# Kernel optimization log

Measured on AMD Instinct MI355X. Metric: run time of the kernel, lower is better.

The kernel has to match this reference:

```python
import jax, jax.numpy as jnp
import numpy as np

NUM_SEG = 196  # fixed max number of segments (fill_max of segment ids)


def setup_inputs() -> dict:
    key = jax.random.key(0)
    ks = jax.random.split(key, 6)
    B, H, W = 16, 224, 224
    in_chans, inter_dim, embed_dim, k = 3, 64, 768, 7
    x = jax.random.normal(ks[0], (B, in_chans, H, W), jnp.float32)
    segment = jax.random.randint(ks[1], (B, H, W), 0, NUM_SEG, dtype=jnp.int64)
    conv1_w = jax.random.normal(ks[2], (inter_dim, in_chans, k, k), jnp.float32) * 0.02
    conv1_b = jnp.zeros((inter_dim,), jnp.float32)
    pos_embed = jax.random.normal(ks[3], (1, inter_dim, H, W), jnp.float32) * 0.02
    conv2_w = jax.random.normal(ks[4], (embed_dim, inter_dim, 3), jnp.float32) * 0.02
    conv2_b = jnp.zeros((embed_dim,), jnp.float32)
    return {"x": x, "segment": segment, "conv1_w": conv1_w, "conv1_b": conv1_b,
            "pos_embed": pos_embed, "conv2_w": conv2_w, "conv2_b": conv2_b}


def _remap(s):
    # torch.unique(return_inverse=True): map ids to ranks in sorted unique order.
    present = jnp.zeros((NUM_SEG,), jnp.int32).at[s].set(1)
    rank = jnp.cumsum(present) - 1  # rank of each possible id among present ids
    return rank[s]


def _segment_mean(hc, idx):
    # hc: [C, N], idx: [N] -> [C, NUM_SEG]; empty segments -> 0 (sum 0 / clamp 1)
    sums = jax.ops.segment_sum(hc.T, idx, num_segments=NUM_SEG)           # [S, C]
    cnt = jax.ops.segment_sum(jnp.ones(idx.shape, hc.dtype), idx,
                              num_segments=NUM_SEG)                       # [S]
    return (sums / jnp.maximum(cnt, 1.0)[:, None]).T


def reference(x, segment, conv1_w, conv1_b, pos_embed, conv2_w, conv2_b):
    # conv1, stride 1, 'same' padding (odd kernel -> SAME matches torch)
    h = jax.lax.conv_general_dilated(
        x, conv1_w, window_strides=(1, 1), padding='SAME',
        dimension_numbers=('NCHW', 'OIHW', 'NCHW')) + conv1_b[None, :, None, None]
    h = h + pos_embed
    B, C, H, W = h.shape
    # segment already at (H, W): nearest-interpolate to same size is identity
    seg = segment.reshape(B, -1).astype(jnp.int32)      # [B, H*W]
    f_segment = jax.vmap(_remap)(seg)                   # per-sample unique inverse
    pooled = jax.vmap(_segment_mean)(h.reshape(B, C, -1), f_segment)  # [B, C, S]
    # conv1d k=3, padding=1
    out = jax.lax.conv_general_dilated(
        pooled, conv2_w, window_strides=(1,), padding=[(1, 1)],
        dimension_numbers=('NCH', 'OIH', 'NCH')) + conv2_b[None, :, None]
    out = out.transpose(0, 2, 1)                        # [B, S, embed_dim]
    return out, f_segment.reshape(B, 1, H, W)
```

## Files before the change

kernel.cpp:

```cpp
#include <hip/hip_runtime.h>
#include <hip/hip_bf16.h>

constexpr int B = 16, H = 224, W = 224, CI = 3, CO = 64, K = 7;
constexpr int SEG = 196, E = 768;
constexpr int HW = H * W;
constexpr int PP = 201;
constexpr int EC = 32;

constexpr int TSLOTS = 10;
constexpr int TROW = 72;
constexpr int TX = 32;

typedef __attribute__((ext_vector_type(8))) short bf16x8;
typedef __attribute__((ext_vector_type(16))) float f32x16;

__device__ inline unsigned short bfb(float f) {
    union { __hip_bfloat16 h; unsigned short u; } cv; cv.h = __float2bfloat16(f); return cv.u;
}
__device__ inline unsigned pack2(float lo, float hi) {
    return (unsigned)bfb(lo) | ((unsigned)bfb(hi) << 16);
}
__device__ inline float bf2f(unsigned short u) {
    return __uint_as_float(((unsigned)u) << 16);
}

__global__ void k_count(const int* __restrict__ seg, int* __restrict__ present,
                        unsigned* __restrict__ counts_raw) {
    __shared__ unsigned cnt[SEG];
    const int tid = threadIdx.x, b = blockIdx.y, y0 = blockIdx.x * 8;
    for (int i = tid; i < SEG; i += 256) cnt[i] = 0u;
    __syncthreads();
    for (int i = tid; i < 8 * W; i += 256) {
        int s = seg[b * HW + y0 * W + i];
        present[b * SEG + s] = 1;
        atomicAdd(&cnt[s], 1u);
    }
    __syncthreads();
    for (int i = tid; i < SEG; i += 256)
        if (cnt[i]) atomicAdd(&counts_raw[b * SEG + i], cnt[i]);
}

__global__ void k_offsets(const int* __restrict__ present,
                          const unsigned* __restrict__ counts_raw,
                          int* __restrict__ rank, int* __restrict__ off_rank,
                          int* __restrict__ cnt_rank, unsigned* __restrict__ cursor) {
    __shared__ int buf[256];
    const int b = blockIdx.x, t = threadIdx.x;
    int pres = (t < SEG) ? present[b * SEG + t] : 0;
    int cv   = (t < SEG) ? (int)counts_raw[b * SEG + t] : 0;
    buf[t] = pres; __syncthreads();
    for (int off = 1; off < 256; off <<= 1) {
        int u = (t >= off) ? buf[t - off] : 0; __syncthreads();
        buf[t] += u; __syncthreads();
    }
    int rk = buf[t] - 1;
    if (t < SEG) rank[b * SEG + t] = rk;
    __syncthreads();
    buf[t] = cv; __syncthreads();
    for (int off = 1; off < 256; off <<= 1) {
        int u = (t >= off) ? buf[t - off] : 0; __syncthreads();
        buf[t] += u; __syncthreads();
    }
    int offx = buf[t] - cv;
    if (t < SEG) {
        cursor[b * SEG + t] = (unsigned)offx;
        cnt_rank[b * SEG + t] = 0;
        off_rank[b * SEG + t] = 0;
    }
    __syncthreads();
    if (t < SEG && pres) {
        cnt_rank[b * SEG + rk] = cv;
        off_rank[b * SEG + rk] = offx;
    }
}

__global__ void k_scatter(const int* __restrict__ seg, const int* __restrict__ rank,
                          unsigned* __restrict__ cursor, unsigned* __restrict__ bucket,
                          float* __restrict__ out2) {
    __shared__ unsigned bcnt[SEG];
    __shared__ int base_l[SEG];
    __shared__ int rank_lds[SEG];
    __shared__ unsigned char ss[8 * W];
    __shared__ unsigned short lp[8 * W];
    const int tid = threadIdx.x, b = blockIdx.y, y0 = blockIdx.x * 8;
    for (int i = tid; i < SEG; i += 256) { bcnt[i] = 0u; rank_lds[i] = rank[b * SEG + i]; }
    __syncthreads();
    for (int i = tid; i < 8 * W; i += 256) {
        int s = seg[b * HW + y0 * W + i];
        ss[i] = (unsigned char)s;
        out2[b * HW + y0 * W + i] = (float)rank_lds[s];
        lp[i] = (unsigned short)atomicAdd(&bcnt[s], 1u);
    }
    __syncthreads();
    for (int i = tid; i < SEG; i += 256)
        if (bcnt[i]) base_l[i] = (int)atomicAdd(&cursor[b * SEG + i], bcnt[i]);
    __syncthreads();
    for (int i = tid; i < 8 * W; i += 256) {
        int s = ss[i];
        bucket[b * HW + base_l[s] + lp[i]] = (unsigned)(y0 * W + i);
    }
}

__global__ void k_post(const float* __restrict__ pos, unsigned short* __restrict__ pos_t) {
    const int p = blockIdx.x * 256 + threadIdx.x;
    unsigned d[32];
    #pragma unroll
    for (int c = 0; c < 32; ++c) {
        float v0 = pos[(size_t)(2 * c) * HW + p];
        float v1 = pos[(size_t)(2 * c + 1) * HW + p];
        d[c] = pack2(v0, v1);
    }
    uint4* op = (uint4*)&pos_t[(size_t)p * 64];
    #pragma unroll
    for (int q = 0; q < 8; ++q) {
        uint4 v = {d[4 * q], d[4 * q + 1], d[4 * q + 2], d[4 * q + 3]};
        op[q] = v;
    }
}

__launch_bounds__(256, 2)
__global__ void k_conv_mfma(const float* __restrict__ x,
                            const float* __restrict__ w1,
                            const float* __restrict__ b1,
                            const unsigned short* __restrict__ pos_t,
                            __hip_bfloat16* __restrict__ h, int b0) {
    __shared__ unsigned short Tl[TSLOTS * TX * TROW];
    __shared__ unsigned short Wl[7 * 32 * 64];

    const int tid = threadIdx.x;
    const int lb  = blockIdx.x;
    const int b   = b0 + lb;
    const int x0  = blockIdx.y * 32;
    const int y0  = blockIdx.z * 28;
    const int lane = tid & 63;
    const int ln31 = lane & 31;
    const int g    = lane >> 5;

    for (int i = tid; i < TSLOTS * TX * TROW; i += 256) Tl[i] = 0;
    for (int i = tid; i < 7 * 32 * 64; i += 256) Wl[i] = 0;
    __syncthreads();

    for (int i = tid; i < CO * CI * K * K; i += 256) {
        int co = i / 147, rem = i % 147;
        int ci = rem / 49, kyx = rem % 49;
        int ky = kyx / 7, kx = kyx % 7;
        Wl[(ky * 32 + ci * 8 + kx) * 64 + co] = bfb(w1[i]);
    }

    auto build = [&](int rbase, int nrows) {
        for (int idx = tid; idx < 96 * nrows; idx += 256) {
            int j = idx / 96, rem = idx % 96;
            int ci = rem >> 5, xl = rem & 31;
            int r = rbase + j;
            unsigned slot = (unsigned)(r + 3) % TSLOTS;
            unsigned d0 = 0, d1 = 0, d2 = 0, d3 = 0;
            if (r >= 0 && r < H) {
                const float* xr = &x[((size_t)(b * CI + ci) * H + r) * W];
                float v[7];
                #pragma unroll
                for (int kx = 0; kx < 7; ++kx) {
                    int gx = x0 + xl - 3 + kx;
                    v[kx] = (gx >= 0 && gx < W) ? xr[gx] : 0.f;
                }
                d0 = pack2(v[0], v[1]); d1 = pack2(v[2], v[3]);
                d2 = pack2(v[4], v[5]); d3 = pack2(v[6], 0.f);
            }
            uint4 dv = {d0, d1, d2, d3};
            *(uint4*)&Tl[(slot * TX + xl) * TROW + ci * 8] = dv;
        }
    };

    build(y0 - 3, TSLOTS);
    __syncthreads();

    bf16x8 bfr[7][2][2];
    #pragma unroll
    for (int ky = 0; ky < 7; ++ky)
        #pragma unroll
        for (int ks = 0; ks < 2; ++ks)
            #pragma unroll
            for (int cg = 0; cg < 2; ++cg) {
                bf16x8 f;
                #pragma unroll
                for (int e = 0; e < 8; ++e)
                    f[e] = (short)Wl[(ky * 32 + ks * 16 + g * 8 + e) * 64 + cg * 32 + ln31];
                bfr[ky][ks][cg] = f;
            }
    const float b1v0 = b1[ln31];
    const float b1v1 = b1[32 + ln31];

    for (int s = 0; s < 7; ++s) {
        const int ys = y0 + s * 4;
        const int y  = ys + (tid >> 6);

        f32x16 c0 = {0.f}; f32x16 c1 = {0.f};
        #pragma unroll
        for (int i = 0; i < 16; ++i) { c0[i] = 0.f; c1[i] = 0.f; }

        #pragma unroll
        for (int ky = 0; ky < 7; ++ky) {
            unsigned slot = (unsigned)(y + ky) % TSLOTS;
            const unsigned short* trow = &Tl[slot * TX * TROW];
            #pragma unroll
            for (int ks = 0; ks < 2; ++ks) {
                bf16x8 a = *(const bf16x8*)&trow[ln31 * TROW + ks * 16 + g * 8];
                c0 = __builtin_amdgcn_mfma_f32_32x32x16_bf16(a, bfr[ky][ks][0], c0, 0, 0, 0);
                c1 = __builtin_amdgcn_mfma_f32_32x32x16_bf16(a, bfr[ky][ks][1], c1, 0, 0, 0);
            }
        }

        #pragma unroll
        for (int reg = 0; reg < 16; ++reg) {
            int pxl = (reg & 3) + 8 * (reg >> 2) + 4 * g;
            size_t p = (size_t)y * W + x0 + pxl;
            float pv0 = bf2f(pos_t[p * 64 + ln31]);
            float pv1 = bf2f(pos_t[p * 64 + 32 + ln31]);
            __hip_bfloat16* hp = &h[((size_t)lb * HW + p) * CO];
            hp[ln31]      = __float2bfloat16(c0[reg] + pv0 + b1v0);
            hp[32 + ln31] = __float2bfloat16(c1[reg] + pv1 + b1v1);
        }

        __syncthreads();
        if (s < 6) build(ys + 7, 4);
        __syncthreads();
    }
}

__global__ void k_gather(const __hip_bfloat16* __restrict__ h,
                         const unsigned* __restrict__ bucket,
                         const int* __restrict__ off_rank,
                         const int* __restrict__ cnt_rank,
                         float* __restrict__ pooled, int b0) {
    const int tid = threadIdx.x;
    const int wave = tid >> 6, lane = tid & 63;
    const int r = blockIdx.x * 4 + wave;
    const int lb = blockIdx.y, b = b0 + lb;
    const int n = cnt_rank[b * SEG + r];
    const int base = off_rank[b * SEG + r];
    const int ps = lane >> 3, cg = lane & 7;

    float acc[8] = {0.f, 0.f, 0.f, 0.f, 0.f, 0.f, 0.f, 0.f};
    const unsigned* bk = &bucket[b * HW + base];
    const int iters = (n + 7) >> 3;
    for (int i = 0; i < iters; ++i) {
        int idx = i * 8 + ps;
        if (idx < n) {
            unsigned p = bk[idx];
            uint4 u = *(const uint4*)&h[((size_t)lb * HW + p) * CO + cg * 8];
            acc[0] += __uint_as_float((u.x & 0xffffu) << 16);
            acc[1] += __uint_as_float(u.x & 0xffff0000u);
            acc[2] += __uint_as_float((u.y & 0xffffu) << 16);
            acc[3] += __uint_as_float(u.y & 0xffff0000u);
            acc[4] += __uint_as_float((u.z & 0xffffu) << 16);
            acc[5] += __uint_as_float(u.z & 0xffff0000u);
            acc[6] += __uint_as_float((u.w & 0xffffu) << 16);
            acc[7] += __uint_as_float(u.w & 0xffff0000u);
        }
    }
    #pragma unroll
    for (int m = 8; m < 64; m <<= 1)
        #pragma unroll
        for (int j = 0; j < 8; ++j) acc[j] += __shfl_xor(acc[j], m, 64);

    if (ps == 0) {
        float inv = (n > 0) ? 1.f / (float)n : 0.f;
        float* op = &pooled[((size_t)b * SEG + r) * CO + cg * 8];
        float4 v0 = {acc[0] * inv, acc[1] * inv, acc[2] * inv, acc[3] * inv};
        float4 v1 = {acc[4] * inv, acc[5] * inv, acc[6] * inv, acc[7] * inv};
        *(float4*)&op[0] = v0;
        *(float4*)&op[4] = v1;
    }
}

__launch_bounds__(256, 2)
__global__ void k_pool_conv1d(const float* __restrict__ pooledg,
                              const float* __restrict__ w2,
                              const float* __restrict__ b2,
                              float* __restrict__ out0) {
    __shared__ float pooled[CO * PP];
    __shared__ float w2l[192 * (EC + 1)];
    const int tid = threadIdx.x;
    const int b  = blockIdx.y;
    const int e0 = blockIdx.x * EC;

    for (int i = tid; i < SEG * CO; i += 256) {
        int s = i >> 6, c = i & 63;
        pooled[c * PP + s + 1] = pooledg[((size_t)b * SEG + s) * CO + c];
    }
    for (int i = tid; i < CO * 5; i += 256) {
        int c = i / 5, hh = i % 5;
        pooled[c * PP + (hh == 0 ? 0 : 196 + hh)] = 0.f;
    }
    for (int i = tid; i < EC * 192; i += 256) {
        int e = i / 192, k = i % 192;
        w2l[k * (EC + 1) + e] = w2[(size_t)(e0 + e) * 192 + k];
    }
    __syncthreads();

    const int txs = tid & 31;
    const int te  = tid >> 5;
    const int s0  = txs * 7;
    float acc[7][4];
    #pragma unroll
    for (int ss = 0; ss < 7; ++ss)
        #pragma unroll
        for (int ee = 0; ee < 4; ++ee) acc[ss][ee] = b2[e0 + te * 4 + ee];

    if (s0 < SEG) {
        #pragma unroll 4
        for (int c = 0; c < CO; ++c) {
            float pv[9];
            #pragma unroll
            for (int j = 0; j < 9; ++j) pv[j] = pooled[c * PP + s0 + j];
            #pragma unroll
            for (int dk = 0; dk < 3; ++dk) {
                float wv[4];
                #pragma unroll
                for (int ee = 0; ee < 4; ++ee)
                    wv[ee] = w2l[(c * 3 + dk) * (EC + 1) + te * 4 + ee];
                #pragma unroll
                for (int ss = 0; ss < 7; ++ss)
                    #pragma unroll
                    for (int ee = 0; ee < 4; ++ee)
                        acc[ss][ee] = fmaf(pv[ss + dk], wv[ee], acc[ss][ee]);
            }
        }
        #pragma unroll
        for (int ss = 0; ss < 7; ++ss) {
            int s = s0 + ss;
            float* op = &out0[((size_t)(b * SEG + s) * E) + e0 + te * 4];
            float4 v0 = {acc[ss][0], acc[ss][1], acc[ss][2], acc[ss][3]};
            *(float4*)op = v0;
        }
    }
}

extern "C" void kernel_launch(void* const* d_in, const int* in_sizes, int n_in,
                              void* d_out, int out_size, void* d_ws, size_t ws_size,
                              hipStream_t stream) {
    const float* x   = (const float*)d_in[0];
    const int*   seg = (const int*)d_in[1];
    const float* w1  = (const float*)d_in[2];
    const float* b1  = (const float*)d_in[3];
    const float* pos = (const float*)d_in[4];
    const float* w2  = (const float*)d_in[5];
    const float* b2  = (const float*)d_in[6];

    float* out0 = (float*)d_out;
    float* out2 = out0 + (size_t)B * SEG * E;

    int*      present    = (int*)d_ws;
    unsigned* counts_raw = (unsigned*)(present + B * SEG);
    int*      rank       = (int*)(counts_raw + B * SEG);
    int*      off_rank   = rank + B * SEG;
    int*      cnt_rank   = off_rank + B * SEG;
    unsigned* cursor     = (unsigned*)(cnt_rank + B * SEG);
    float*    pooled     = (float*)(cursor + B * SEG);
    unsigned* bucket     = (unsigned*)(pooled + (size_t)B * SEG * CO);
    unsigned short* pos_t = (unsigned short*)(bucket + (size_t)B * HW);
    __hip_bfloat16* hbuf = (__hip_bfloat16*)(pos_t + (size_t)HW * CO);

    hipMemsetAsync(d_ws, 0, (size_t)2 * B * SEG * 4, stream);

    k_post   <<<dim3(HW / 256), 256, 0, stream>>>(pos, pos_t);
    k_count  <<<dim3(28, B), 256, 0, stream>>>(seg, present, counts_raw);
    k_offsets<<<dim3(B),     256, 0, stream>>>(present, counts_raw, rank, off_rank, cnt_rank, cursor);
    k_scatter<<<dim3(28, B), 256, 0, stream>>>(seg, rank, cursor, bucket, out2);

    size_t used = (char*)hbuf - (char*)d_ws;
    size_t h_per_img = (size_t)HW * CO * sizeof(__hip_bfloat16);
    size_t avail = (ws_size > used) ? ws_size - used : 0;
    int ipc = (int)(avail / h_per_img);
    if (ipc < 1) ipc = 1;
    if (ipc > B) ipc = B;

    for (int b0 = 0; b0 < B; b0 += ipc) {
        int nb = (b0 + ipc <= B) ? ipc : (B - b0);
        k_conv_mfma<<<dim3(nb, 7, 8), 256, 0, stream>>>(x, w1, b1, pos_t, hbuf, b0);
        k_gather   <<<dim3(49, nb),   256, 0, stream>>>(hbuf, bucket, off_rank, cnt_rank, pooled, b0);
    }
    k_pool_conv1d<<<dim3(24, B), 256, 0, stream>>>(pooled, w2, b2, out0);
}
```

Before: 248.5 us.

## Pre-pack conv weights, fold bias into pos, prefetch input rows across MFMA steps

Moves the conv1 weight transpose into a small kernel that writes weights already laid out as MFMA B fragments, so each conv block loads them with vector loads and no longer needs the weight LDS array. The bias is folded into the pre-transposed positional embedding. The input tile gets a compact LDS layout, which frees shared memory and lets the launch bound rise to 3 blocks per SM. Next-row input loads are issued into registers before the MFMA loop and written to LDS after it, so global latency overlaps compute. The cost is higher register pressure from the prefetch buffers and one extra kernel launch.

```diff
diff --git a/kernel.cpp b/kernel.cpp
--- a/kernel.cpp
+++ b/kernel.cpp
@@ -8,8 +8,6 @@
 constexpr int EC = 32;
 
 constexpr int TSLOTS = 10;
-constexpr int TROW = 72;
-constexpr int TX = 32;
 
 typedef __attribute__((ext_vector_type(8))) short bf16x8;
 typedef __attribute__((ext_vector_type(16))) float f32x16;
@@ -101,13 +99,14 @@
     }
 }
 
-__global__ void k_post(const float* __restrict__ pos, unsigned short* __restrict__ pos_t) {
+__global__ void k_post(const float* __restrict__ pos, const float* __restrict__ b1,
+                       unsigned short* __restrict__ pos_t) {
     const int p = blockIdx.x * 256 + threadIdx.x;
     unsigned d[32];
     #pragma unroll
     for (int c = 0; c < 32; ++c) {
-        float v0 = pos[(size_t)(2 * c) * HW + p];
-        float v1 = pos[(size_t)(2 * c + 1) * HW + p];
+        float v0 = pos[(size_t)(2 * c) * HW + p]     + b1[2 * c];
+        float v1 = pos[(size_t)(2 * c + 1) * HW + p] + b1[2 * c + 1];
         d[c] = pack2(v0, v1);
     }
     uint4* op = (uint4*)&pos_t[(size_t)p * 64];
@@ -118,14 +117,27 @@
     }
 }
 
-__launch_bounds__(256, 2)
+__global__ void k_wt(const float* __restrict__ w1, unsigned short* __restrict__ w1t) {
+    int i = blockIdx.x * 256 + threadIdx.x;
+    if (i < 7 * 2 * 2 * 64 * 8) {
+        int e = i & 7, lane = (i >> 3) & 63, cg = (i >> 9) & 1, ks = (i >> 10) & 1, ky = i >> 11;
+        int kk = ks * 16 + (lane >> 5) * 8 + e;
+        int co = cg * 32 + (lane & 31);
+        float v = 0.f;
+        if (kk < 24) {
+            int ci = kk >> 3, kx = kk & 7;
+            if (kx < 7) v = w1[((co * 3 + ci) * 7 + ky) * 7 + kx];
+        }
+        w1t[i] = bfb(v);
+    }
+}
+
+__launch_bounds__(256, 3)
 __global__ void k_conv_mfma(const float* __restrict__ x,
-                            const float* __restrict__ w1,
-                            const float* __restrict__ b1,
+                            const unsigned short* __restrict__ w1t,
                             const unsigned short* __restrict__ pos_t,
                             __hip_bfloat16* __restrict__ h, int b0) {
-    __shared__ unsigned short Tl[TSLOTS * TX * TROW];
-    __shared__ unsigned short Wl[7 * 32 * 64];
+    __shared__ unsigned short Tl[TSLOTS * 4 * 32 * 8];
 
     const int tid = threadIdx.x;
     const int lb  = blockIdx.x;
@@ -135,43 +147,7 @@
     const int lane = tid & 63;
     const int ln31 = lane & 31;
     const int g    = lane >> 5;
-
-    for (int i = tid; i < TSLOTS * TX * TROW; i += 256) Tl[i] = 0;
-    for (int i = tid; i < 7 * 32 * 64; i += 256) Wl[i] = 0;
-    __syncthreads();
-
-    for (int i = tid; i < CO * CI * K * K; i += 256) {
-        int co = i / 147, rem = i % 147;
-        int ci = rem / 49, kyx = rem % 49;
-        int ky = kyx / 7, kx = kyx % 7;
-        Wl[(ky * 32 + ci * 8 + kx) * 64 + co] = bfb(w1[i]);
-    }
-
-    auto build = [&](int rbase, int nrows) {
-        for (int idx = tid; idx < 96 * nrows; idx += 256) {
-            int j = idx / 96, rem = idx % 96;
-            int ci = rem >> 5, xl = rem & 31;
-            int r = rbase + j;
-            unsigned slot = (unsigned)(r + 3) % TSLOTS;
-            unsigned d0 = 0, d1 = 0, d2 = 0, d3 = 0;
-            if (r >= 0 && r < H) {
-                const float* xr = &x[((size_t)(b * CI + ci) * H + r) * W];
-                float v[7];
-                #pragma unroll
-                for (int kx = 0; kx < 7; ++kx) {
-                    int gx = x0 + xl - 3 + kx;
-                    v[kx] = (gx >= 0 && gx < W) ? xr[gx] : 0.f;
-                }
-                d0 = pack2(v[0], v[1]); d1 = pack2(v[2], v[3]);
-                d2 = pack2(v[4], v[5]); d3 = pack2(v[6], 0.f);
-            }
-            uint4 dv = {d0, d1, d2, d3};
-            *(uint4*)&Tl[(slot * TX + xl) * TROW + ci * 8] = dv;
-        }
-    };
-
-    build(y0 - 3, TSLOTS);
-    __syncthreads();
+    const int wave = tid >> 6;
 
     bf16x8 bfr[7][2][2];
     #pragma unroll
@@ -179,49 +155,111 @@
         #pragma unroll
         for (int ks = 0; ks < 2; ++ks)
             #pragma unroll
-            for (int cg = 0; cg < 2; ++cg) {
-                bf16x8 f;
-                #pragma unroll
-                for (int e = 0; e < 8; ++e)
-                    f[e] = (short)Wl[(ky * 32 + ks * 16 + g * 8 + e) * 64 + cg * 32 + ln31];
-                bfr[ky][ks][cg] = f;
-            }
-    const float b1v0 = b1[ln31];
-    const float b1v1 = b1[32 + ln31];
+            for (int cg = 0; cg < 2; ++cg)
+                bfr[ky][ks][cg] = *(const bf16x8*)&w1t[((((ky * 2 + ks) * 2 + cg) * 64) + lane) * 8];
+
+    for (int i = tid; i < TSLOTS * 4 * 32 * 8; i += 256) Tl[i] = 0;
+    __syncthreads();
+    for (int idx = tid; idx < 96 * TSLOTS; idx += 256) {
+        int jr = idx / 96, rem = idx % 96;
+        int ci = rem >> 5, xl = rem & 31;
+        int r = y0 - 3 + jr;
+        unsigned slot = (unsigned)(r + 3) % TSLOTS;
+        uint4 dv = {0, 0, 0, 0};
+        if (r >= 0 && r < H) {
+            const float* xr = &x[((size_t)(b * CI + ci) * H + r) * W];
+            float v[7];
+            #pragma unroll
+            for (int kx = 0; kx < 7; ++kx) {
+                int gx = x0 + xl - 3 + kx;
+                v[kx] = (gx >= 0 && gx < W) ? xr[gx] : 0.f;
+            }
+            dv.x = pack2(v[0], v[1]); dv.y = pack2(v[2], v[3]);
+            dv.z = pack2(v[4], v[5]); dv.w = pack2(v[6], 0.f);
+        }
+        *(uint4*)&Tl[((slot * 4 + ci) * 32 + xl) * 8] = dv;
+    }
+    __syncthreads();
 
     for (int s = 0; s < 7; ++s) {
         const int ys = y0 + s * 4;
-        const int y  = ys + (tid >> 6);
-
-        f32x16 c0 = {0.f}; f32x16 c1 = {0.f};
+        const int y  = ys + wave;
+
+        float ld0[7], ld1[7];
+        int slot0 = 0, slot1 = 0, ci0 = 0, ci1 = 0, xl0 = 0, xl1 = 0;
+        bool act1 = false;
+        if (s < 6) {
+            {
+                int idx = tid;
+                int jr = idx / 96, rem = idx % 96;
+                ci0 = rem >> 5; xl0 = rem & 31;
+                int r = ys + 7 + jr;
+                slot0 = (int)((unsigned)(r + 3) % TSLOTS);
+                #pragma unroll
+                for (int kx = 0; kx < 7; ++kx) {
+                    int gx = x0 + xl0 - 3 + kx;
+                    bool ok = (r < H) && gx >= 0 && gx < W;
+                    ld0[kx] = ok ? x[((size_t)(b * CI + ci0) * H + r) * W + gx] : 0.f;
+                }
+            }
+            {
+                int idx = tid + 256;
+                act1 = idx < 384;
+                int jr = idx / 96, rem = idx % 96;
+                ci1 = rem >> 5; xl1 = rem & 31;
+                int r = ys + 7 + jr;
+                slot1 = (int)((unsigned)(r + 3) % TSLOTS);
+                #pragma unroll
+                for (int kx = 0; kx < 7; ++kx) {
+                    int gx = x0 + xl1 - 3 + kx;
+                    bool ok = act1 && (r < H) && gx >= 0 && gx < W;
+                    ld1[kx] = ok ? x[((size_t)(b * CI + ci1) * H + r) * W + gx] : 0.f;
+                }
+            }
+        }
+
+        f32x16 c0, c1;
         #pragma unroll
         for (int i = 0; i < 16; ++i) { c0[i] = 0.f; c1[i] = 0.f; }
-
+        int sl = y % TSLOTS;
         #pragma unroll
         for (int ky = 0; ky < 7; ++ky) {
-            unsigned slot = (unsigned)(y + ky) % TSLOTS;
-            const unsigned short* trow = &Tl[slot * TX * TROW];
-            #pragma unroll
-            for (int ks = 0; ks < 2; ++ks) {
-                bf16x8 a = *(const bf16x8*)&trow[ln31 * TROW + ks * 16 + g * 8];
-                c0 = __builtin_amdgcn_mfma_f32_32x32x16_bf16(a, bfr[ky][ks][0], c0, 0, 0, 0);
-                c1 = __builtin_amdgcn_mfma_f32_32x32x16_bf16(a, bfr[ky][ks][1], c1, 0, 0, 0);
-            }
+            const unsigned short* tq = &Tl[sl * (4 * 32 * 8)];
+            bf16x8 a0 = *(const bf16x8*)&tq[((0 * 2 + g) * 32 + ln31) * 8];
+            bf16x8 a1 = *(const bf16x8*)&tq[((1 * 2 + g) * 32 + ln31) * 8];
+            c0 = __builtin_amdgcn_mfma_f32_32x32x16_bf16(a0, bfr[ky][0][0], c0, 0, 0, 0);
+            c1 = __builtin_amdgcn_mfma_f32_32x32x16_bf16(a0, bfr[ky][0][1], c1, 0, 0, 0);
+            c0 = __builtin_amdgcn_mfma_f32_32x32x16_bf16(a1, bfr[ky][1][0], c0, 0, 0, 0);
+            c1 = __builtin_amdgcn_mfma_f32_32x32x16_bf16(a1, bfr[ky][1][1], c1, 0, 0, 0);
+            sl = (sl + 1 == TSLOTS) ? 0 : sl + 1;
         }
 
         #pragma unroll
         for (int reg = 0; reg < 16; ++reg) {
             int pxl = (reg & 3) + 8 * (reg >> 2) + 4 * g;
-            size_t p = (size_t)y * W + x0 + pxl;
-            float pv0 = bf2f(pos_t[p * 64 + ln31]);
-            float pv1 = bf2f(pos_t[p * 64 + 32 + ln31]);
+            int p = y * W + x0 + pxl;
+            float pv0 = bf2f(pos_t[(size_t)p * 64 + ln31]);
+            float pv1 = bf2f(pos_t[(size_t)p * 64 + 32 + ln31]);
             __hip_bfloat16* hp = &h[((size_t)lb * HW + p) * CO];
-            hp[ln31]      = __float2bfloat16(c0[reg] + pv0 + b1v0);
-            hp[32 + ln31] = __float2bfloat16(c1[reg] + pv1 + b1v1);
+            hp[ln31]      = __float2bfloat16(c0[reg] + pv0);
+            hp[32 + ln31] = __float2bfloat16(c1[reg] + pv1);
         }
 
         __syncthreads();
-        if (s < 6) build(ys + 7, 4);
+        if (s < 6) {
+            {
+                uint4 dv;
+                dv.x = pack2(ld0[0], ld0[1]); dv.y = pack2(ld0[2], ld0[3]);
+                dv.z = pack2(ld0[4], ld0[5]); dv.w = pack2(ld0[6], 0.f);
+                *(uint4*)&Tl[((slot0 * 4 + ci0) * 32 + xl0) * 8] = dv;
+            }
+            if (act1) {
+                uint4 dv;
+                dv.x = pack2(ld1[0], ld1[1]); dv.y = pack2(ld1[2], ld1[3]);
+                dv.z = pack2(ld1[4], ld1[5]); dv.w = pack2(ld1[6], 0.f);
+                *(uint4*)&Tl[((slot1 * 4 + ci1) * 32 + xl1) * 8] = dv;
+            }
+        }
         __syncthreads();
     }
 }
@@ -358,11 +396,13 @@
     float*    pooled     = (float*)(cursor + B * SEG);
     unsigned* bucket     = (unsigned*)(pooled + (size_t)B * SEG * CO);
     unsigned short* pos_t = (unsigned short*)(bucket + (size_t)B * HW);
-    __hip_bfloat16* hbuf = (__hip_bfloat16*)(pos_t + (size_t)HW * CO);
+    unsigned short* w1t  = pos_t + (size_t)HW * CO;
+    __hip_bfloat16* hbuf = (__hip_bfloat16*)(w1t + 7 * 2 * 2 * 64 * 8);
 
     hipMemsetAsync(d_ws, 0, (size_t)2 * B * SEG * 4, stream);
 
-    k_post   <<<dim3(HW / 256), 256, 0, stream>>>(pos, pos_t);
+    k_post   <<<dim3(HW / 256), 256, 0, stream>>>(pos, b1, pos_t);
+    k_wt     <<<dim3(56),       256, 0, stream>>>(w1, w1t);
     k_count  <<<dim3(28, B), 256, 0, stream>>>(seg, present, counts_raw);
     k_offsets<<<dim3(B),     256, 0, stream>>>(present, counts_raw, rank, off_rank, cnt_rank, cursor);
     k_scatter<<<dim3(28, B), 256, 0, stream>>>(seg, rank, cursor, bucket, out2);
@@ -376,7 +416,7 @@
 
     for (int b0 = 0; b0 < B; b0 += ipc) {
         int nb = (b0 + ipc <= B) ? ipc : (B - b0);
-        k_conv_mfma<<<dim3(nb, 7, 8), 256, 0, stream>>>(x, w1, b1, pos_t, hbuf, b0);
+        k_conv_mfma<<<dim3(nb, 7, 8), 256, 0, stream>>>(x, w1t, pos_t, hbuf, b0);
         k_gather   <<<dim3(49, nb),   256, 0, stream>>>(hbuf, bucket, off_rank, cnt_rank, pooled, b0);
     }
     k_pool_conv1d<<<dim3(24, B), 256, 0, stream>>>(pooled, w2, b2, out0);
```

New measurement: 352.5 us. +41.9%, slower.
